# Kernel tuning notes

Hardware: AMD Instinct MI355X
Metric: run time of the kernel (lower is better)

The kernel has to match this reference:

```python
import jax, jax.numpy as jnp
import numpy as np

D_MODEL = 1024
B, N = 8, 2048

def setup_inputs() -> dict:
    key = jax.random.key(0)
    k1, k2, k3 = jax.random.split(key, 3)
    x = jax.random.normal(k1, (B, N, D_MODEL), dtype=jnp.float32)
    W_qkv = jax.random.normal(k2, (3 * D_MODEL, D_MODEL), dtype=jnp.float32) * (D_MODEL ** -0.5)
    b_qkv = jax.random.normal(k3, (3 * D_MODEL,), dtype=jnp.float32) * 0.02
    return {"x": x, "W_qkv": W_qkv, "b_qkv": b_qkv}

def reference(x, W_qkv, b_qkv):
    d = x.shape[-1]
    scale = d ** 0.5
    # qkv projection: torch Linear computes x @ W.T + b
    qkv = jnp.einsum('bnc,oc->bno', x, W_qkv) + b_qkv  # [B, N, 3d]
    q, k, v = jnp.split(qkv, 3, axis=-1)               # each [B, N, d]
    scores = jnp.einsum('bqd,bkd->bqk', q, k) / scale  # [B, N, N]
    attn = jax.nn.softmax(scores, axis=-1)
    return jnp.einsum('bqk,bkd->bqd', attn, v)         # [B, N, d]
```

## Files before the change

### kernel.cpp

```cpp
#include <hip/hip_runtime.h>


#define AS1 __attribute__((address_space(1)))
#define AS3 __attribute__((address_space(3)))

typedef __bf16 bfrag  __attribute__((ext_vector_type(8)));
typedef float  ffrag  __attribute__((ext_vector_type(4)));
typedef __bf16 bf16x4 __attribute__((ext_vector_type(4)));

__global__ __launch_bounds__(256) void cvt_fused(const float* __restrict__ x,
                                                 const float* __restrict__ W,
                                                 __bf16* __restrict__ xb,
                                                 __bf16* __restrict__ Wb,
                                                 float* __restrict__ rowsum) {
  const int gid = blockIdx.x * 256 + threadIdx.x;
  const int stride = gridDim.x * 256;
  for (int k = gid; k < 4194304; k += stride) {
    float4 v = ((const float4*)x)[k];
    bf16x4 o;
    o[0] = (__bf16)v.x; o[1] = (__bf16)v.y; o[2] = (__bf16)v.z; o[3] = (__bf16)v.w;
    ((bf16x4*)xb)[k] = o;
  }
  for (int k = gid; k < 786432; k += stride) {
    float4 v = ((const float4*)W)[k];
    bf16x4 o;
    o[0] = (__bf16)v.x; o[1] = (__bf16)v.y; o[2] = (__bf16)v.z; o[3] = (__bf16)v.w;
    ((bf16x4*)Wb)[k] = o;
  }
  for (int k = gid; k < 16384; k += stride) rowsum[k] = 0.0f;
}

__device__ __forceinline__ void stage_half(
    const __bf16* __restrict__ Atile, const __bf16* __restrict__ Btile,
    int lda, int ldb, __bf16* lds, int tid, int te, int h) {
  const int kt = te * 64;
  const __bf16* src = (h < 2) ? Atile : Btile;
  const int ld = (h < 2) ? lda : ldb;
  const int row0 = (h & 1) * 128;
  __bf16* dst = lds + (te & 1) * 32768 + h * 8192;
#pragma unroll
  for (int l = 0; l < 2; ++l) {
    const int y = l * 4096 + tid * 8;
    const int r = y >> 6;
    const int c = ((tid & 7) * 8) ^ ((r & 7) << 3);
    __builtin_amdgcn_global_load_lds((AS1 void*)(src + (size_t)(row0 + r) * ld + kt + c),
                                     (AS3 void*)(dst + y), 16, 0, 0);
  }
}

template <int QA>
__device__ __forceinline__ void rd_a(const __bf16* lds, int bufoff, int aRowBase,
                                     int ck0, int ck1, bfrag a[4][2]) {
#pragma unroll
  for (int m = 0; m < 4; ++m) {
    const int off = bufoff + aRowBase + QA * 8192 + m * 1024;
    a[m][0] = *(const bfrag*)&lds[off + ck0];
    a[m][1] = *(const bfrag*)&lds[off + ck1];
  }
}

template <int QB>
__device__ __forceinline__ void rd_bq(const __bf16* lds, int bufoff, int bRowBase,
                                      int ck0, int ck1, bfrag b[2][2]) {
#pragma unroll
  for (int n = 0; n < 2; ++n) {
    const int off = bufoff + bRowBase + QB * 8192 + n * 1024;
    b[n][0] = *(const bfrag*)&lds[off + ck0];
    b[n][1] = *(const bfrag*)&lds[off + ck1];
  }
}

#define PH(QA, QB, BREG, DOVM)                                                 \
  {                                                                            \
    if (DOVM) asm volatile("s_waitcnt vmcnt(6)" ::: "memory");                 \
    __builtin_amdgcn_s_barrier();                                              \
    asm volatile("s_waitcnt lgkmcnt(0)" ::: "memory");                         \
    __builtin_amdgcn_s_setprio(1);                                             \
    _Pragma("unroll") for (int m_ = 0; m_ < 4; ++m_)                           \
    _Pragma("unroll") for (int n_ = 0; n_ < 2; ++n_)                           \
    _Pragma("unroll") for (int ks_ = 0; ks_ < 2; ++ks_)                        \
      acc[(QA) * 4 + m_][(QB) * 2 + n_] =                                      \
          __builtin_amdgcn_mfma_f32_16x16x32_bf16(                             \
              a[m_][ks_], BREG[n_][ks_], acc[(QA) * 4 + m_][(QB) * 2 + n_],    \
              0, 0, 0);                                                        \
    __builtin_amdgcn_s_setprio(0);                                             \
    __builtin_amdgcn_s_barrier();                                              \
    __builtin_amdgcn_sched_barrier(0);                                         \
  }

#define STG(TE, H) stage_half(Atile, Btile, lda, ldb, lds, tid, (TE), (H))

__device__ __forceinline__ void gemm256_mainloop(
    const __bf16* __restrict__ Atile, const __bf16* __restrict__ Btile,
    int lda, int ldb, int K, __bf16* lds, ffrag acc[8][4]) {
  const int tid  = threadIdx.x;
  const int lane = tid & 63;
  const int wid  = tid >> 6;
  const int wr   = wid >> 2, wc = wid & 3;
  const int fr   = lane & 15;
  const int fk   = (lane >> 4) * 8;
  const int swz  = (fr & 7) << 3;
  const int ck0  = fk ^ swz;
  const int ck1  = (32 + fk) ^ swz;
  const int aRowBase = (wr * 64 + fr) * 64;
  const int bRowBase = 16384 + (wc * 32 + fr) * 64;
  const int nT = K >> 6;

  STG(0, 0); STG(0, 2); STG(0, 3); STG(0, 1);
  STG(1, 0); STG(1, 2); STG(1, 3);
  asm volatile("s_waitcnt vmcnt(6)" ::: "memory");
  __builtin_amdgcn_s_barrier();

  const int nIter = nT >> 1;
#pragma unroll 1
  for (int i = 0; i < nIter; ++i) {
    const int t1  = 2 * i + 1;
    const int t2e = (2 * i + 2 < nT) ? (2 * i + 2) : (2 * i);
    const int t3e = (2 * i + 3 < nT) ? (2 * i + 3) : (2 * i + 1);
    bfrag a[4][2], b0f[2][2], b1f[2][2];
    rd_a<0>(lds, 0, aRowBase, ck0, ck1, a);
    rd_bq<0>(lds, 0, bRowBase, ck0, ck1, b0f);
    STG(t1, 1);
    PH(0, 0, b0f, false)
    rd_bq<1>(lds, 0, bRowBase, ck0, ck1, b1f);
    STG(t2e, 0);
    PH(0, 1, b1f, false)
    rd_a<1>(lds, 0, aRowBase, ck0, ck1, a);
    STG(t2e, 2);
    PH(1, 1, b1f, false)
    STG(t2e, 3);
    PH(1, 0, b0f, true)
    rd_a<0>(lds, 32768, aRowBase, ck0, ck1, a);
    rd_bq<0>(lds, 32768, bRowBase, ck0, ck1, b0f);
    STG(t2e, 1);
    PH(0, 0, b0f, false)
    rd_bq<1>(lds, 32768, bRowBase, ck0, ck1, b1f);
    STG(t3e, 0);
    PH(0, 1, b1f, false)
    rd_a<1>(lds, 32768, aRowBase, ck0, ck1, a);
    STG(t3e, 2);
    PH(1, 1, b1f, false)
    STG(t3e, 3);
    PH(1, 0, b0f, true)
  }
}

#define ACC_ZERO()                                                             \
  ffrag acc[8][4];                                                             \
  _Pragma("unroll") for (int m = 0; m < 8; ++m)                                \
  _Pragma("unroll") for (int n = 0; n < 4; ++n) acc[m][n] = (ffrag)(0.0f);


__global__ __launch_bounds__(512, 2) void qkv_gemm256(
    const __bf16* __restrict__ Abf, const __bf16* __restrict__ Wbf,
    const float* __restrict__ bias,
    __bf16* __restrict__ Q, __bf16* __restrict__ Ko, __bf16* __restrict__ Vt) {
  __shared__ __bf16 lds[65536];
  ACC_ZERO();
  int bid = (int)blockIdx.x;
  bid = (bid & 7) * 96 + (bid >> 3);
  const int brow = (bid / 12) * 256;
  const int bcol = (bid % 12) * 256;
  gemm256_mainloop(Abf + (size_t)brow * 1024, Wbf + (size_t)bcol * 1024,
                   1024, 1024, 1024, lds, acc);
  const int lane = threadIdx.x & 63, wid = threadIdx.x >> 6;
  const int wr = wid >> 2, wc = wid & 3;
  const int region = bcol >> 10;
  if (region < 2) {
    __bf16* dst = region == 0 ? Q : Ko;
    const float scale = region == 0 ? 0.03125f : 1.0f;
#pragma unroll
    for (int j = 0; j < 4; ++j) {
      const int qb = j >> 1, n = j & 1;
      const int col = bcol + qb * 128 + wc * 32 + n * 16 + (lane & 15);
      const int o = col & 1023;
      const float bv = bias[col];
#pragma unroll
      for (int i = 0; i < 8; ++i) {
        const int qa = i >> 2, m = i & 3;
#pragma unroll
        for (int r = 0; r < 4; ++r) {
          const int mg = brow + qa * 128 + wr * 64 + m * 16 + (lane >> 4) * 4 + r;
          dst[(size_t)mg * 1024 + o] = (__bf16)((acc[i][j][r] + bv) * scale);
        }
      }
    }
  } else {
#pragma unroll
    for (int j = 0; j < 4; ++j) {
      const int qb = j >> 1, n = j & 1;
      const int col = bcol + qb * 128 + wc * 32 + n * 16 + (lane & 15);
      const int o = col & 1023;
      const float bv = bias[col];
#pragma unroll
      for (int i = 0; i < 8; ++i) {
        const int qa = i >> 2, m = i & 3;
        const int mg0 = brow + qa * 128 + wr * 64 + m * 16 + (lane >> 4) * 4;
        const int b = mg0 >> 11, nr = mg0 & 2047;
        bf16x4 v;
#pragma unroll
        for (int r = 0; r < 4; ++r) v[r] = (__bf16)(acc[i][j][r] + bv);
        *(bf16x4*)&Vt[(size_t)b * 2097152 + (size_t)o * 2048 + nr] = v;
      }
    }
  }
}

__global__ __launch_bounds__(512, 2) void scores_gemm256(const __bf16* __restrict__ Q,
                                                         const __bf16* __restrict__ Kb,
                                                         __bf16* __restrict__ Pu,
                                                         float* __restrict__ rowsum) {
  __shared__ __bf16 lds[65536];
  ACC_ZERO();
  int bid = (int)blockIdx.x;
  const int wg = (bid & 7) * 64 + (bid >> 3);
  const int brow = (wg & 7) * 256, bcol = ((wg >> 3) & 7) * 256, z = wg >> 6;
  gemm256_mainloop(Q + (size_t)z * 2048 * 1024 + (size_t)brow * 1024,
                   Kb + (size_t)z * 2048 * 1024 + (size_t)bcol * 1024,
                   1024, 1024, 1024, lds, acc);
  const int lane = threadIdx.x & 63, wid = threadIdx.x >> 6;
  const int wr = wid >> 2, wc = wid & 3;
  const int fr = lane & 15, g4 = (lane >> 4) * 4;
#pragma unroll
  for (int i = 0; i < 8; ++i) {
    const int qa = i >> 2, m = i & 3;
#pragma unroll
    for (int r = 0; r < 4; ++r) {
      const int mg = brow + qa * 128 + wr * 64 + m * 16 + g4 + r;
      float part = 0.0f;
#pragma unroll
      for (int j = 0; j < 4; ++j) {
        const int qb = j >> 1, n = j & 1;
        const int o = bcol + qb * 128 + wc * 32 + n * 16 + fr;
        const float e = __expf(acc[i][j][r] - 16.0f);
        part += e;
        Pu[((size_t)(z * 2048 + mg)) * 2048 + o] = (__bf16)e;
      }
      part += __shfl_xor(part, 1, 64);
      part += __shfl_xor(part, 2, 64);
      part += __shfl_xor(part, 4, 64);
      part += __shfl_xor(part, 8, 64);
      if (fr == 0) atomicAdd(&rowsum[z * 2048 + mg], part);
    }
  }
}

__global__ __launch_bounds__(512, 2) void pv_gemm256(const __bf16* __restrict__ P,
                                                     const __bf16* __restrict__ Vt,
                                                     const float* __restrict__ rowsum,
                                                     float* __restrict__ O) {
  __shared__ __bf16 lds[65536];
  ACC_ZERO();
  int bid = (int)blockIdx.x;
  const int wg = (bid & 7) * 32 + (bid >> 3);
  const int brow = (wg & 7) * 256, bcol = ((wg >> 3) & 3) * 256, z = wg >> 5;
  gemm256_mainloop(P + (size_t)(z * 2048 + brow) * 2048,
                   Vt + (size_t)z * 1024 * 2048 + (size_t)bcol * 2048,
                   2048, 2048, 2048, lds, acc);
  const int lane = threadIdx.x & 63, wid = threadIdx.x >> 6;
  const int wr = wid >> 2, wc = wid & 3;
  const int fr = lane & 15, g4 = (lane >> 4) * 4;
#pragma unroll
  for (int i = 0; i < 8; ++i) {
    const int qa = i >> 2, m = i & 3;
#pragma unroll
    for (int r = 0; r < 4; ++r) {
      const int mg = brow + qa * 128 + wr * 64 + m * 16 + g4 + r;
      const float inv = 1.0f / rowsum[z * 2048 + mg];
#pragma unroll
      for (int j = 0; j < 4; ++j) {
        const int qb = j >> 1, n = j & 1;
        const int o = bcol + qb * 128 + wc * 32 + n * 16 + fr;
        O[((size_t)(z * 2048 + mg)) * 1024 + o] = acc[i][j][r] * inv;
      }
    }
  }
}

extern "C" void kernel_launch(void* const* d_in, const int* in_sizes, int n_in,
                              void* d_out, int out_size, void* d_ws, size_t ws_size,
                              hipStream_t stream) {
  (void)in_sizes; (void)n_in; (void)out_size; (void)ws_size;
  const float* x    = (const float*)d_in[0];
  const float* W    = (const float*)d_in[1];
  const float* bias = (const float*)d_in[2];
  float* out = (float*)d_out;
  char* ws = (char*)d_ws;
  const size_t MB = 1u << 20;
  __bf16* x_bf = (__bf16*)(ws + 0);
  __bf16* W_bf = (__bf16*)(ws + 32 * MB);
  __bf16* Qb   = (__bf16*)(ws + 38 * MB);
  __bf16* Kb   = (__bf16*)(ws + 70 * MB);
  __bf16* Pu   = (__bf16*)(ws + 102 * MB);
  __bf16* Vt   = (__bf16*)(ws + 166 * MB);
  float* rowsum = (float*)(ws + 198 * MB);

  cvt_fused<<<2048, 256, 0, stream>>>(x, W, x_bf, W_bf, rowsum);
  qkv_gemm256<<<768, 512, 0, stream>>>(x_bf, W_bf, bias, Qb, Kb, Vt);
  scores_gemm256<<<512, 512, 0, stream>>>(Qb, Kb, Pu, rowsum);
  pv_gemm256<<<256, 512, 0, stream>>>(Pu, Vt, rowsum, out);
}
```

Baseline: 256.5 us.

## Make QKV and scores GEMM blocks loop over multiple output tiles sharing A rows

The QKV projection now launches 256 blocks, and each block computes the Q, K and V tiles for the same 256-row slice of x in sequence. The scores kernel also launches 256 blocks, each computing two column tiles for the same Q row slice. Both kernels map blocks to XCDs explicitly so a block's A tile stays hot in cache between iterations, and the launch count roughly matches one wave on the device. The trade-off is fewer, longer blocks with serialized mainloops, which can give a worse tail and less latency hiding.

After: 313.9 us. +22.4%, slower.

```diff
diff --git a/kernel.cpp b/kernel.cpp
--- a/kernel.cpp
+++ b/kernel.cpp
@@ -145,8 +145,7 @@
   }
 }
 
-#define ACC_ZERO()                                                             \
-  ffrag acc[8][4];                                                             \
+#define ACC_CLEAR()                                                            \
   _Pragma("unroll") for (int m = 0; m < 8; ++m)                                \
   _Pragma("unroll") for (int n = 0; n < 4; ++n) acc[m][n] = (ffrag)(0.0f);
 
@@ -156,51 +155,54 @@
     const float* __restrict__ bias,
     __bf16* __restrict__ Q, __bf16* __restrict__ Ko, __bf16* __restrict__ Vt) {
   __shared__ __bf16 lds[65536];
-  ACC_ZERO();
-  int bid = (int)blockIdx.x;
-  bid = (bid & 7) * 96 + (bid >> 3);
-  const int brow = (bid / 12) * 256;
-  const int bcol = (bid % 12) * 256;
-  gemm256_mainloop(Abf + (size_t)brow * 1024, Wbf + (size_t)bcol * 1024,
-                   1024, 1024, 1024, lds, acc);
+  ffrag acc[8][4];
+  const int bid = (int)blockIdx.x;
+  const int xcd = bid & 7, li = bid >> 3;
+  const int brow = (xcd * 8 + (li >> 2)) * 256;
+  const int ocol = (li & 3) * 256;
   const int lane = threadIdx.x & 63, wid = threadIdx.x >> 6;
   const int wr = wid >> 2, wc = wid & 3;
-  const int region = bcol >> 10;
-  if (region < 2) {
-    __bf16* dst = region == 0 ? Q : Ko;
-    const float scale = region == 0 ? 0.03125f : 1.0f;
-#pragma unroll
-    for (int j = 0; j < 4; ++j) {
-      const int qb = j >> 1, n = j & 1;
-      const int col = bcol + qb * 128 + wc * 32 + n * 16 + (lane & 15);
-      const int o = col & 1023;
-      const float bv = bias[col];
-#pragma unroll
-      for (int i = 0; i < 8; ++i) {
-        const int qa = i >> 2, m = i & 3;
-#pragma unroll
-        for (int r = 0; r < 4; ++r) {
-          const int mg = brow + qa * 128 + wr * 64 + m * 16 + (lane >> 4) * 4 + r;
-          dst[(size_t)mg * 1024 + o] = (__bf16)((acc[i][j][r] + bv) * scale);
+  const __bf16* Atile = Abf + (size_t)brow * 1024;
+
+#pragma unroll 1
+  for (int reg = 0; reg < 3; ++reg) {
+    ACC_CLEAR();
+    gemm256_mainloop(Atile, Wbf + (size_t)(reg * 1024 + ocol) * 1024,
+                     1024, 1024, 1024, lds, acc);
+    if (reg < 2) {
+      __bf16* dst = reg == 0 ? Q : Ko;
+      const float scale = reg == 0 ? 0.03125f : 1.0f;
+#pragma unroll
+      for (int j = 0; j < 4; ++j) {
+        const int qb = j >> 1, n = j & 1;
+        const int o = ocol + qb * 128 + wc * 32 + n * 16 + (lane & 15);
+        const float bv = bias[reg * 1024 + o];
+#pragma unroll
+        for (int i = 0; i < 8; ++i) {
+          const int qa = i >> 2, m = i & 3;
+#pragma unroll
+          for (int r = 0; r < 4; ++r) {
+            const int mg = brow + qa * 128 + wr * 64 + m * 16 + (lane >> 4) * 4 + r;
+            dst[(size_t)mg * 1024 + o] = (__bf16)((acc[i][j][r] + bv) * scale);
+          }
         }
       }
-    }
-  } else {
-#pragma unroll
-    for (int j = 0; j < 4; ++j) {
-      const int qb = j >> 1, n = j & 1;
-      const int col = bcol + qb * 128 + wc * 32 + n * 16 + (lane & 15);
-      const int o = col & 1023;
-      const float bv = bias[col];
-#pragma unroll
-      for (int i = 0; i < 8; ++i) {
-        const int qa = i >> 2, m = i & 3;
-        const int mg0 = brow + qa * 128 + wr * 64 + m * 16 + (lane >> 4) * 4;
-        const int b = mg0 >> 11, nr = mg0 & 2047;
-        bf16x4 v;
-#pragma unroll
-        for (int r = 0; r < 4; ++r) v[r] = (__bf16)(acc[i][j][r] + bv);
-        *(bf16x4*)&Vt[(size_t)b * 2097152 + (size_t)o * 2048 + nr] = v;
+    } else {
+#pragma unroll
+      for (int j = 0; j < 4; ++j) {
+        const int qb = j >> 1, n = j & 1;
+        const int o = ocol + qb * 128 + wc * 32 + n * 16 + (lane & 15);
+        const float bv = bias[2048 + o];
+#pragma unroll
+        for (int i = 0; i < 8; ++i) {
+          const int qa = i >> 2, m = i & 3;
+          const int mg0 = brow + qa * 128 + wr * 64 + m * 16 + (lane >> 4) * 4;
+          const int b = mg0 >> 11, nr = mg0 & 2047;
+          bf16x4 v;
+#pragma unroll
+          for (int r = 0; r < 4; ++r) v[r] = (__bf16)(acc[i][j][r] + bv);
+          *(bf16x4*)&Vt[(size_t)b * 2097152 + (size_t)o * 2048 + nr] = v;
+        }
       }
     }
   }
@@ -211,36 +213,42 @@
                                                          __bf16* __restrict__ Pu,
                                                          float* __restrict__ rowsum) {
   __shared__ __bf16 lds[65536];
-  ACC_ZERO();
-  int bid = (int)blockIdx.x;
-  const int wg = (bid & 7) * 64 + (bid >> 3);
-  const int brow = (wg & 7) * 256, bcol = ((wg >> 3) & 7) * 256, z = wg >> 6;
-  gemm256_mainloop(Q + (size_t)z * 2048 * 1024 + (size_t)brow * 1024,
-                   Kb + (size_t)z * 2048 * 1024 + (size_t)bcol * 1024,
-                   1024, 1024, 1024, lds, acc);
+  ffrag acc[8][4];
+  const int bid = (int)blockIdx.x;
+  const int z = bid & 7, li = bid >> 3;
+  const int brow = (li >> 2) * 256;
   const int lane = threadIdx.x & 63, wid = threadIdx.x >> 6;
   const int wr = wid >> 2, wc = wid & 3;
   const int fr = lane & 15, g4 = (lane >> 4) * 4;
-#pragma unroll
-  for (int i = 0; i < 8; ++i) {
-    const int qa = i >> 2, m = i & 3;
-#pragma unroll
-    for (int r = 0; r < 4; ++r) {
-      const int mg = brow + qa * 128 + wr * 64 + m * 16 + g4 + r;
-      float part = 0.0f;
-#pragma unroll
-      for (int j = 0; j < 4; ++j) {
-        const int qb = j >> 1, n = j & 1;
-        const int o = bcol + qb * 128 + wc * 32 + n * 16 + fr;
-        const float e = __expf(acc[i][j][r] - 16.0f);
-        part += e;
-        Pu[((size_t)(z * 2048 + mg)) * 2048 + o] = (__bf16)e;
+  const __bf16* Atile = Q + (size_t)z * 2048 * 1024 + (size_t)brow * 1024;
+
+#pragma unroll 1
+  for (int half = 0; half < 2; ++half) {
+    const int bcol = ((li & 3) + half * 4) * 256;
+    ACC_CLEAR();
+    gemm256_mainloop(Atile, Kb + (size_t)z * 2048 * 1024 + (size_t)bcol * 1024,
+                     1024, 1024, 1024, lds, acc);
+#pragma unroll
+    for (int i = 0; i < 8; ++i) {
+      const int qa = i >> 2, m = i & 3;
+#pragma unroll
+      for (int r = 0; r < 4; ++r) {
+        const int mg = brow + qa * 128 + wr * 64 + m * 16 + g4 + r;
+        float part = 0.0f;
+#pragma unroll
+        for (int j = 0; j < 4; ++j) {
+          const int qb = j >> 1, n = j & 1;
+          const int o = bcol + qb * 128 + wc * 32 + n * 16 + fr;
+          const float e = __expf(acc[i][j][r] - 16.0f);
+          part += e;
+          Pu[((size_t)(z * 2048 + mg)) * 2048 + o] = (__bf16)e;
+        }
+        part += __shfl_xor(part, 1, 64);
+        part += __shfl_xor(part, 2, 64);
+        part += __shfl_xor(part, 4, 64);
+        part += __shfl_xor(part, 8, 64);
+        if (fr == 0) atomicAdd(&rowsum[z * 2048 + mg], part);
       }
-      part += __shfl_xor(part, 1, 64);
-      part += __shfl_xor(part, 2, 64);
-      part += __shfl_xor(part, 4, 64);
-      part += __shfl_xor(part, 8, 64);
-      if (fr == 0) atomicAdd(&rowsum[z * 2048 + mg], part);
     }
   }
 }
@@ -250,7 +258,8 @@
                                                      const float* __restrict__ rowsum,
                                                      float* __restrict__ O) {
   __shared__ __bf16 lds[65536];
-  ACC_ZERO();
+  ffrag acc[8][4];
+  ACC_CLEAR();
   int bid = (int)blockIdx.x;
   const int wg = (bid & 7) * 32 + (bid >> 3);
   const int brow = (wg & 7) * 256, bcol = ((wg >> 3) & 3) * 256, z = wg >> 5;
@@ -296,7 +305,7 @@
   float* rowsum = (float*)(ws + 198 * MB);
 
   cvt_fused<<<2048, 256, 0, stream>>>(x, W, x_bf, W_bf, rowsum);
-  qkv_gemm256<<<768, 512, 0, stream>>>(x_bf, W_bf, bias, Qb, Kb, Vt);
-  scores_gemm256<<<512, 512, 0, stream>>>(Qb, Kb, Pu, rowsum);
+  qkv_gemm256<<<256, 512, 0, stream>>>(x_bf, W_bf, bias, Qb, Kb, Vt);
+  scores_gemm256<<<256, 512, 0, stream>>>(Qb, Kb, Pu, rowsum);
   pv_gemm256<<<256, 512, 0, stream>>>(Pu, Vt, rowsum, out);
 }
```
